# Kernel optimization log

Hardware: AMD Instinct MI355X
Metric: run time of the kernel (lower is better)

Reference implementation:

```python
import jax, jax.numpy as jnp
import numpy as np

N = 2048        # batch (nodes/edges)
DIM = 512       # irreps dim for x, y, and output
C = 16          # channel multiplicity
NNZ = 4096      # number of sparse CG paths


def setup_inputs() -> dict:
    key = jax.random.key(0)
    k1, k2, k3, k4, k5, k6 = jax.random.split(key, 6)
    x = jax.random.normal(k1, (N, DIM, C), dtype=jnp.float32)
    y = jax.random.normal(k2, (N, DIM, C), dtype=jnp.float32)
    scale = jax.random.normal(k3, (NNZ,), dtype=jnp.float32)
    index1 = jax.random.randint(k4, (NNZ,), 0, DIM)
    index2 = jax.random.randint(k5, (NNZ,), 0, DIM)
    index_out = jnp.sort(jax.random.randint(k6, (NNZ,), 0, DIM))
    return {"x": x, "y": y, "scale": scale,
            "index1": index1, "index2": index2, "index_out": index_out,
            "out_size": DIM}


def reference(x, y, scale, index1, index2, index_out, out_size):
    # gather both operands along the irreps dim  -> [N, NNZ, C]
    inter = scale[None, :, None] * x[:, index1, :] * y[:, index2, :]
    # scatter-add (segment + scatter in the original, fused here since
    # segment-then-scatter over disjoint segments == one scatter-add)
    out = jnp.zeros((x.shape[0], out_size, x.shape[-1]), dtype=x.dtype)
    out = out.at[:, index_out, :].add(inter)  # [N, out_size, C]
    return out
```

## Files before the change

### kernel.cpp

```cpp
#include <hip/hip_runtime.h>

constexpr int DIM = 512;
constexpr int C   = 16;
constexpr int TPB = 1024;
constexpr int STRIDE = 20;
constexpr int LDSF = DIM * STRIDE;
constexpr int GROUPS = TPB / 4;

__global__ __launch_bounds__(1024) void setup_kernel(
    const int* __restrict__ io,
    const int* __restrict__ i1,
    const int* __restrict__ i2,
    const float* __restrict__ scale,
    int4* __restrict__ plan,
    int4* __restrict__ pdata,
    int nnz) {
    if (blockIdx.x == 0) {
        __shared__ int s_start[DIM + 1];
        __shared__ int s_len[DIM];
        const int t = threadIdx.x;
        if (t <= DIM) {
            int lo = 0, hi = nnz;
            while (lo < hi) {
                int mid = (lo + hi) >> 1;
                if (io[mid] < t) lo = mid + 1; else hi = mid;
            }
            s_start[t] = lo;
        }
        __syncthreads();
        if (t < DIM) s_len[t] = s_start[t + 1] - s_start[t];
        __syncthreads();
        if (t < DIM) {
            const int ld = s_len[t];
            int rank = 0;
            #pragma unroll 8
            for (int j = 0; j < DIM; ++j) {
                const int lj = s_len[j];
                rank += (lj > ld) || (lj == ld && j < t);
            }
            plan[rank] = make_int4(s_start[t], s_start[t + 1], t * C, 0);
        }
    } else {
        const int p = (blockIdx.x - 1) * 1024 + threadIdx.x;
        if (p < nnz)
            pdata[p] = make_int4(i1[p] * STRIDE, i2[p] * STRIDE,
                                 __float_as_int(scale[p]), 0);
    }
}

__global__ __launch_bounds__(TPB) void tp_kernel(
    const float* __restrict__ x, const float* __restrict__ y,
    const int4* __restrict__ plan,
    const int4* __restrict__ pdata,
    float* __restrict__ out) {
    extern __shared__ float lds[];
    float* xs = lds;
    float* ys = lds + LDSF;
    float4* xs4 = reinterpret_cast<float4*>(xs);
    float4* ys4 = reinterpret_cast<float4*>(ys);

    const int n = blockIdx.x;
    const float4* __restrict__ xg = reinterpret_cast<const float4*>(x) + (size_t)n * (DIM * C / 4);
    const float4* __restrict__ yg = reinterpret_cast<const float4*>(y) + (size_t)n * (DIM * C / 4);

    #pragma unroll
    for (int s = threadIdx.x; s < DIM * 4; s += TPB) {
        const int slot = (s >> 2) * 5 + (s & 3);
        xs4[slot] = xg[s];
        ys4[slot] = yg[s];
    }
    __syncthreads();

    const int l4  = threadIdx.x & 3;
    const int grp = threadIdx.x >> 2;
    const int c4f = l4 * 4;
    float* __restrict__ obase = out + (size_t)n * (DIM * C) + c4f;

    #pragma unroll
    for (int k = 0; k < 2; ++k) {
        const int4 pl = plan[k ? (DIM - 1 - grp) : grp];
        const int s = pl.x;
        const int e = pl.y;
        float ax = 0.f, ay = 0.f, az = 0.f, aw = 0.f;
        if (s < e) {
            const int last = e - 1;
            int4   pd0 = pdata[s];
            int4   pd1 = pdata[s + 1 < last ? s + 1 : last];
            float4 xv0 = *reinterpret_cast<const float4*>(xs + pd0.x + c4f);
            float4 yv0 = *reinterpret_cast<const float4*>(ys + pd0.y + c4f);
            float4 xv1 = *reinterpret_cast<const float4*>(xs + pd1.x + c4f);
            float4 yv1 = *reinterpret_cast<const float4*>(ys + pd1.y + c4f);
            for (int p = s; p < e; ++p) {
                const int    pn  = p + 2 < last ? p + 2 : last;
                const int4   pd2 = pdata[pn];
                const float4 xv2 = *reinterpret_cast<const float4*>(xs + pd2.x + c4f);
                const float4 yv2 = *reinterpret_cast<const float4*>(ys + pd2.y + c4f);
                const float  sc  = __int_as_float(pd0.z);
                ax = fmaf(sc * xv0.x, yv0.x, ax);
                ay = fmaf(sc * xv0.y, yv0.y, ay);
                az = fmaf(sc * xv0.z, yv0.z, az);
                aw = fmaf(sc * xv0.w, yv0.w, aw);
                pd0 = pd1; pd1 = pd2;
                xv0 = xv1; xv1 = xv2;
                yv0 = yv1; yv1 = yv2;
            }
        }
        *reinterpret_cast<float4*>(obase + pl.z) = make_float4(ax, ay, az, aw);
    }
}

extern "C" void kernel_launch(void* const* d_in, const int* in_sizes, int n_in,
                              void* d_out, int out_size, void* d_ws, size_t ws_size,
                              hipStream_t stream) {
    const float* x     = (const float*)d_in[0];
    const float* y     = (const float*)d_in[1];
    const float* scale = (const float*)d_in[2];
    const int*   i1    = (const int*)d_in[3];
    const int*   i2    = (const int*)d_in[4];
    const int*   io    = (const int*)d_in[5];
    float* out = (float*)d_out;

    const int nnz = in_sizes[2];
    const int N   = in_sizes[0] / (DIM * C);

    int4* plan  = (int4*)d_ws;
    int4* pdata = (int4*)((char*)d_ws + 8192);

    const int pack_blocks = (nnz + 1023) / 1024;
    setup_kernel<<<1 + pack_blocks, 1024, 0, stream>>>(io, i1, i2, scale, plan, pdata, nnz);

    constexpr size_t lds_bytes = (size_t)2 * LDSF * sizeof(float);
    (void)hipFuncSetAttribute((const void*)tp_kernel,
                              hipFuncAttributeMaxDynamicSharedMemorySize,
                              (int)lds_bytes);
    tp_kernel<<<N, TPB, lds_bytes, stream>>>(x, y, plan, pdata, out);
}
```

Baseline: 81.41 us.

## Store x/y tiles in LDS as bf16, shrink blocks to 256 threads, deeper prefetch

Converts the staged x and y rows to packed bf16 in shared memory, which halves LDS use per block (about 40KB). It also drops the block to 256 threads, each handling 8 output rows in a zigzag order over the sorted plan. Plan entries and the heads of the path lists are prefetched one or two rows ahead, and path metadata is pipelined four deep. The aim is higher occupancy and overlap of global loads, at the cost of bf16 rounding error in the products, which may exceed tolerance.

```diff
diff --git a/kernel.cpp b/kernel.cpp
--- a/kernel.cpp
+++ b/kernel.cpp
@@ -2,10 +2,9 @@
 
 constexpr int DIM = 512;
 constexpr int C   = 16;
-constexpr int TPB = 1024;
-constexpr int STRIDE = 20;
-constexpr int LDSF = DIM * STRIDE;
-constexpr int GROUPS = TPB / 4;
+constexpr int TPB = 256;
+constexpr int USTRIDE = 10;
+constexpr int BUFU = DIM * USTRIDE;
 
 __global__ __launch_bounds__(1024) void setup_kernel(
     const int* __restrict__ io,
@@ -43,9 +42,33 @@
     } else {
         const int p = (blockIdx.x - 1) * 1024 + threadIdx.x;
         if (p < nnz)
-            pdata[p] = make_int4(i1[p] * STRIDE, i2[p] * STRIDE,
+            pdata[p] = make_int4(i1[p] * USTRIDE, i2[p] * USTRIDE,
                                  __float_as_int(scale[p]), 0);
     }
+}
+
+__device__ __forceinline__ unsigned int pk_bf16(float a, float b) {
+    unsigned int ua = __float_as_uint(a);
+    unsigned int ub = __float_as_uint(b);
+    ua = (ua + 0x7FFFu + ((ua >> 16) & 1u)) >> 16;
+    ub = (ub + 0x7FFFu + ((ub >> 16) & 1u)) & 0xFFFF0000u;
+    return ua | ub;
+}
+
+struct Heads { int4 h0, h1, h2, h3; };
+
+__device__ __forceinline__ Heads load_heads(const int4* __restrict__ pdata,
+                                            int s, int e) {
+    Heads H;
+    H.h0 = H.h1 = H.h2 = H.h3 = make_int4(0, 0, 0, 0);
+    if (s < e) {
+        const int last = e - 1;
+        H.h0 = pdata[s];
+        H.h1 = pdata[s + 1 < last ? s + 1 : last];
+        H.h2 = pdata[s + 2 < last ? s + 2 : last];
+        H.h3 = pdata[s + 3 < last ? s + 3 : last];
+    }
+    return H;
 }
 
 __global__ __launch_bounds__(TPB) void tp_kernel(
@@ -53,11 +76,8 @@
     const int4* __restrict__ plan,
     const int4* __restrict__ pdata,
     float* __restrict__ out) {
-    extern __shared__ float lds[];
-    float* xs = lds;
-    float* ys = lds + LDSF;
-    float4* xs4 = reinterpret_cast<float4*>(xs);
-    float4* ys4 = reinterpret_cast<float4*>(ys);
+    __shared__ unsigned int xs[BUFU];
+    __shared__ unsigned int ys[BUFU];
 
     const int n = blockIdx.x;
     const float4* __restrict__ xg = reinterpret_cast<const float4*>(x) + (size_t)n * (DIM * C / 4);
@@ -65,47 +85,67 @@
 
     #pragma unroll
     for (int s = threadIdx.x; s < DIM * 4; s += TPB) {
-        const int slot = (s >> 2) * 5 + (s & 3);
-        xs4[slot] = xg[s];
-        ys4[slot] = yg[s];
+        const int slot = (s >> 2) * USTRIDE + (s & 3) * 2;
+        const float4 xv = xg[s];
+        const float4 yv = yg[s];
+        *reinterpret_cast<uint2*>(xs + slot) =
+            make_uint2(pk_bf16(xv.x, xv.y), pk_bf16(xv.z, xv.w));
+        *reinterpret_cast<uint2*>(ys + slot) =
+            make_uint2(pk_bf16(yv.x, yv.y), pk_bf16(yv.z, yv.w));
     }
     __syncthreads();
 
     const int l4  = threadIdx.x & 3;
     const int grp = threadIdx.x >> 2;
-    const int c4f = l4 * 4;
-    float* __restrict__ obase = out + (size_t)n * (DIM * C) + c4f;
+    const int cu2 = l4 * 2;
+    float* __restrict__ obase = out + (size_t)n * (DIM * C) + l4 * 4;
+
+    int4 pl  = plan[grp];
+    int4 pln = plan[64 + (63 - grp)];
+    Heads Hc = load_heads(pdata, pl.x, pl.y);
 
     #pragma unroll
-    for (int k = 0; k < 2; ++k) {
-        const int4 pl = plan[k ? (DIM - 1 - grp) : grp];
-        const int s = pl.x;
-        const int e = pl.y;
+    for (int k = 0; k < 8; ++k) {
+        const int rnn = (k + 2 < 8)
+            ? ((k + 2) << 6) + (((k + 2) & 1) ? (63 - grp) : grp) : 0;
+        const int4 plnn = plan[rnn];
+        const Heads Hn = (k + 1 < 8) ? load_heads(pdata, pln.x, pln.y) : Hc;
+
+        const int s = pl.x, e = pl.y;
         float ax = 0.f, ay = 0.f, az = 0.f, aw = 0.f;
         if (s < e) {
             const int last = e - 1;
-            int4   pd0 = pdata[s];
-            int4   pd1 = pdata[s + 1 < last ? s + 1 : last];
-            float4 xv0 = *reinterpret_cast<const float4*>(xs + pd0.x + c4f);
-            float4 yv0 = *reinterpret_cast<const float4*>(ys + pd0.y + c4f);
-            float4 xv1 = *reinterpret_cast<const float4*>(xs + pd1.x + c4f);
-            float4 yv1 = *reinterpret_cast<const float4*>(ys + pd1.y + c4f);
+            uint2 xv0 = *reinterpret_cast<const uint2*>(xs + Hc.h0.x + cu2);
+            uint2 yv0 = *reinterpret_cast<const uint2*>(ys + Hc.h0.y + cu2);
+            uint2 xv1 = *reinterpret_cast<const uint2*>(xs + Hc.h1.x + cu2);
+            uint2 yv1 = *reinterpret_cast<const uint2*>(ys + Hc.h1.y + cu2);
+            float s0 = __int_as_float(Hc.h0.z);
+            float s1 = __int_as_float(Hc.h1.z);
+            int4 q2 = Hc.h2, q3 = Hc.h3;
             for (int p = s; p < e; ++p) {
-                const int    pn  = p + 2 < last ? p + 2 : last;
-                const int4   pd2 = pdata[pn];
-                const float4 xv2 = *reinterpret_cast<const float4*>(xs + pd2.x + c4f);
-                const float4 yv2 = *reinterpret_cast<const float4*>(ys + pd2.y + c4f);
-                const float  sc  = __int_as_float(pd0.z);
-                ax = fmaf(sc * xv0.x, yv0.x, ax);
-                ay = fmaf(sc * xv0.y, yv0.y, ay);
-                az = fmaf(sc * xv0.z, yv0.z, az);
-                aw = fmaf(sc * xv0.w, yv0.w, aw);
-                pd0 = pd1; pd1 = pd2;
-                xv0 = xv1; xv1 = xv2;
-                yv0 = yv1; yv1 = yv2;
+                const int4 q4 = pdata[p + 4 < last ? p + 4 : last];
+                const uint2 xv2 = *reinterpret_cast<const uint2*>(xs + q2.x + cu2);
+                const uint2 yv2 = *reinterpret_cast<const uint2*>(ys + q2.y + cu2);
+                const float x0 = __uint_as_float(xv0.x << 16);
+                const float x1 = __uint_as_float(xv0.x & 0xFFFF0000u);
+                const float x2 = __uint_as_float(xv0.y << 16);
+                const float x3 = __uint_as_float(xv0.y & 0xFFFF0000u);
+                const float y0 = __uint_as_float(yv0.x << 16);
+                const float y1 = __uint_as_float(yv0.x & 0xFFFF0000u);
+                const float y2 = __uint_as_float(yv0.y << 16);
+                const float y3 = __uint_as_float(yv0.y & 0xFFFF0000u);
+                ax = fmaf(s0 * x0, y0, ax);
+                ay = fmaf(s0 * x1, y1, ay);
+                az = fmaf(s0 * x2, y2, az);
+                aw = fmaf(s0 * x3, y3, aw);
+                s0 = s1; s1 = __int_as_float(q2.z);
+                q2 = q3; q3 = q4;
+                xv0 = xv1; yv0 = yv1; xv1 = xv2; yv1 = yv2;
             }
         }
         *reinterpret_cast<float4*>(obase + pl.z) = make_float4(ax, ay, az, aw);
+
+        pl = pln; pln = plnn; Hc = Hn;
     }
 }
 
@@ -128,10 +168,5 @@
 
     const int pack_blocks = (nnz + 1023) / 1024;
     setup_kernel<<<1 + pack_blocks, 1024, 0, stream>>>(io, i1, i2, scale, plan, pdata, nnz);
-
-    constexpr size_t lds_bytes = (size_t)2 * LDSF * sizeof(float);
-    (void)hipFuncSetAttribute((const void*)tp_kernel,
-                              hipFuncAttributeMaxDynamicSharedMemorySize,
-                              (int)lds_bytes);
-    tp_kernel<<<N, TPB, lds_bytes, stream>>>(x, y, plan, pdata, out);
+    tp_kernel<<<N, TPB, 0, stream>>>(x, y, plan, pdata, out);
 }
```

Measured after the change: 83.65 us. +2.7%, slower.
